# Performance work log

Hardware: AMD Instinct MI355X
Metric: run time of the kernel (lower is better)

Reference implementation:

```python
import jax, jax.numpy as jnp
import numpy as np

D = 256          # in_dim == out_dim for both layers
B, S = 8, 1024   # batch, seq_len
EPS = 1e-5       # LayerNorm eps (torch default)


def _layernorm(x, g, b):
    mu = jnp.mean(x, axis=-1, keepdims=True)
    var = jnp.var(x, axis=-1, keepdims=True)
    return (x - mu) * jax.lax.rsqrt(var + EPS) * g + b


def _periods(d):
    i = jnp.arange(d, dtype=jnp.float32)
    # periods[i, j] = i*d + j + 2
    return i[:, None] * d + i[None, :] + 2.0


def _layer(x, M, P, g, b, positions):
    # x: [B, S, in_dim] -> [B, S, out_dim]
    x_trans = jnp.einsum('bsj,ij->bsi', x, M)      # x @ M.T
    x_trans = _layernorm(x_trans, g, b)
    k = positions.astype(jnp.float32)[:, None, None]            # [S,1,1]
    phi = jnp.cos(2.0 * jnp.pi * k / _periods(D)[None])         # [S,D,D]
    Mk = P[None] * phi                                          # [S,D,D]
    Nk = jnp.einsum('bsj,sij->bsi', x_trans, Mk)
    # use_residual='separate' with in_dim==out_dim -> Identity residual
    return Nk + x


def setup_inputs() -> dict:
    key = jax.random.key(0)
    ks = jax.random.split(key, 5)
    seq = jax.random.normal(ks[0], (B, S, D), dtype=jnp.float32)
    M1 = jax.random.uniform(ks[1], (D, D), jnp.float32, -0.5, 0.5)
    P1 = jax.random.uniform(ks[2], (D, D), jnp.float32, -0.1, 0.1)
    M2 = jax.random.uniform(ks[3], (D, D), jnp.float32, -0.5, 0.5)
    P2 = jax.random.uniform(ks[4], (D, D), jnp.float32, -0.1, 0.1)
    g1 = jnp.ones((D,), jnp.float32); b1 = jnp.zeros((D,), jnp.float32)
    g2 = jnp.ones((D,), jnp.float32); b2 = jnp.zeros((D,), jnp.float32)
    return {"seq": seq, "M1": M1, "P1": P1, "g1": g1, "b1": b1,
            "M2": M2, "P2": P2, "g2": g2, "b2": b2}


def reference(seq, M1, P1, g1, b1, M2, P2, g2, b2):
    positions = jnp.arange(S)
    x = _layer(seq, M1, P1, g1, b1, positions)
    x = _layer(x, M2, P2, g2, b2, positions)
    return x
```

## Files before the change

kernel.cpp:

```cpp
#include <hip/hip_runtime.h>

#define DD 256
#define BB 8
#define SS 1024
#define XSTRIDE 264
#define RSTRIDE 260

#define LAYER_BYTES 262144
#define PTAB_OFF    131072
#define WS_NEEDED   (2 * LAYER_BYTES)

typedef _Float16 half8  __attribute__((ext_vector_type(8)));
typedef _Float16 half2t __attribute__((ext_vector_type(2)));
typedef __fp16   fp16x2 __attribute__((ext_vector_type(2)));
typedef __attribute__((ext_vector_type(4))) float float4v;

union h8u { half8 h; half2t h2[4]; };

__device__ __forceinline__ half2t pkrtz(float a, float b) {
    union { fp16x2 f; half2t h; } cv;
    cv.f = __builtin_amdgcn_cvt_pkrtz(a, b);
    return cv.h;
}

__device__ __forceinline__ float cosrev(float x) {
    return __builtin_amdgcn_cosf(__builtin_amdgcn_fractf(x));
}

__global__ void build_tabs(const float* __restrict__ M1, const float* __restrict__ P1,
                           const float* __restrict__ M2, const float* __restrict__ P2,
                           char* __restrict__ ws)
{
    int gid   = blockIdx.x * 256 + threadIdx.x;
    int layer = gid >> 13;
    int gi    = gid & 8191;
    int idx   = gi >> 6;
    int lane  = gi & 63;
    int wt    = idx & 15;
    int l15   = lane & 15, quad = lane >> 4;
    int kt    = idx >> 4;
    int n     = 16 * wt + l15;
    int j0    = kt * 32 + quad * 8;

    const float* Msrc = layer ? M2 : M1;
    const float* Psrc = layer ? P2 : P1;

    h8u mh, ph;
    #pragma unroll
    for (int e = 0; e < 4; ++e) {
        float ma = Msrc[(size_t)n * DD + j0 + 2 * e];
        float mb = Msrc[(size_t)n * DD + j0 + 2 * e + 1];
        float pa = Psrc[(size_t)n * DD + j0 + 2 * e];
        float pb = Psrc[(size_t)n * DD + j0 + 2 * e + 1];
        mh.h2[e] = pkrtz(ma, mb);
        ph.h2[e] = pkrtz(pa, pb);
    }
    char* base = ws + (size_t)layer * LAYER_BYTES;
    ((half8*)base)[gi]              = mh.h;
    ((half8*)(base + PTAB_OFF))[gi] = ph.h;
}

template<bool TABS>
__global__ __launch_bounds__(512, 4)
void fused_hierddpm(const float* __restrict__ seq,
                    const float* __restrict__ M1, const float* __restrict__ P1,
                    const float* __restrict__ g1, const float* __restrict__ be1,
                    const float* __restrict__ M2, const float* __restrict__ P2,
                    const float* __restrict__ g2, const float* __restrict__ be2,
                    const char* __restrict__ ws,
                    float* __restrict__ out)
{
    __shared__ __align__(16) _Float16 xsb[16][XSTRIDE];
    __shared__ __align__(16) _Float16 xtb[16][XSTRIDE];
    __shared__ __align__(16) float2 stats[16][8];
    __shared__ __align__(16) float res_lds[16][RSTRIDE];

    const int tid  = threadIdx.x;
    const int w    = tid >> 6;
    const int lane = tid & 63;
    const int l15  = lane & 15;
    const int quad = lane >> 4;
    const int s0   = blockIdx.x * 2;
    const float k0 = (float)s0;

    {
        const float4* seq4 = (const float4*)seq;
        #pragma unroll
        for (int u = 0; u < 2; ++u) {
            int v  = tid + 512 * u;
            int sl = v >> 9;
            int rm = v & 511;
            int b  = rm >> 6, j4 = rm & 63;
            float4 x = seq4[((size_t)b * SS + s0 + sl) * 64 + j4];
            int r = sl * 8 + b;
            half2t* dst = (half2t*)&xsb[r][4 * j4];
            dst[0] = pkrtz(x.x, x.y);
            dst[1] = pkrtz(x.z, x.w);
            *(float4*)&res_lds[r][4 * j4] = x;
        }
    }
    __syncthreads();

    #pragma unroll 1
    for (int layer = 0; layer < 2; ++layer) {
        const float* M  = layer ? M2  : M1;
        const float* P  = layer ? P2  : P1;
        const float* g  = layer ? g2  : g1;
        const float* be = layer ? be2 : be1;
        const char*  lbase = ws + (size_t)layer * LAYER_BYTES;
        const half8* Mtab = (const half8*)lbase;
        const half8* Ptab = (const half8*)(lbase + PTAB_OFF);

        float4v acc1[2];
        acc1[0] = (float4v){0.f, 0.f, 0.f, 0.f};
        acc1[1] = (float4v){0.f, 0.f, 0.f, 0.f};

        half8 aN = *(const half8*)&xsb[l15][quad * 8];
        half8 b0N, b1N;
        if (TABS) {
            b0N = Mtab[(2 * w) * 64 + lane];
            b1N = Mtab[(2 * w + 1) * 64 + lane];
        }
        #pragma unroll 1
        for (int kt = 0; kt < 8; ++kt) {
            half8 aC = aN;
            half8 b0C, b1C;
            if (TABS) {
                b0C = b0N; b1C = b1N;
            } else {
                #pragma unroll
                for (int t = 0; t < 2; ++t) {
                    int n = 16 * (2 * w + t) + l15;
                    const float4* Mr = (const float4*)M + ((size_t)n * 64 + kt * 8 + quad * 2);
                    float4 m0 = Mr[0], m1 = Mr[1];
                    h8u bb2;
                    bb2.h2[0] = pkrtz(m0.x, m0.y);
                    bb2.h2[1] = pkrtz(m0.z, m0.w);
                    bb2.h2[2] = pkrtz(m1.x, m1.y);
                    bb2.h2[3] = pkrtz(m1.z, m1.w);
                    if (t == 0) b0C = bb2.h; else b1C = bb2.h;
                }
            }
            if (kt < 7) {
                aN = *(const half8*)&xsb[l15][(kt + 1) * 32 + quad * 8];
                if (TABS) {
                    b0N = Mtab[((kt + 1) * 16 + 2 * w) * 64 + lane];
                    b1N = Mtab[((kt + 1) * 16 + 2 * w + 1) * 64 + lane];
                }
            }
            acc1[0] = __builtin_amdgcn_mfma_f32_16x16x32_f16(aC, b0C, acc1[0], 0, 0, 0);
            acc1[1] = __builtin_amdgcn_mfma_f32_16x16x32_f16(aC, b1C, acc1[1], 0, 0, 0);
        }

        half8 p0N, p1N;
        if (TABS) {
            p0N = Ptab[(2 * w) * 64 + lane];
            p1N = Ptab[(2 * w + 1) * 64 + lane];
        }

        #pragma unroll
        for (int reg = 0; reg < 4; ++reg) {
            float v0 = acc1[0][reg], v1 = acc1[1][reg];
            float sm = v0 + v1;
            float sq = fmaf(v0, v0, v1 * v1);
            #pragma unroll
            for (int off = 1; off < 16; off <<= 1) {
                sm += __shfl_xor(sm, off, 64);
                sq += __shfl_xor(sq, off, 64);
            }
            if (l15 == 0) stats[quad * 4 + reg][w] = make_float2(sm, sq);
        }
        __syncthreads();
        {
            int c0i = 16 * (2 * w) + l15, c1i = 16 * (2 * w + 1) + l15;
            float gv0 = g[c0i], bv0 = be[c0i];
            float gv1 = g[c1i], bv1 = be[c1i];
            #pragma unroll
            for (int reg = 0; reg < 4; ++reg) {
                int m = quad * 4 + reg;
                const float4* s4 = (const float4*)&stats[m][0];
                float4 q0 = s4[0], q1 = s4[1], q2 = s4[2], q3 = s4[3];
                float sm = (q0.x + q0.z) + (q1.x + q1.z) + (q2.x + q2.z) + (q3.x + q3.z);
                float sq = (q0.y + q0.w) + (q1.y + q1.w) + (q2.y + q2.w) + (q3.y + q3.w);
                float mm = sm * (1.f / DD);
                float rs = rsqrtf(sq * (1.f / DD) - mm * mm + 1e-5f);
                xtb[m][c0i] = (_Float16)fmaf((acc1[0][reg] - mm) * rs, gv0, bv0);
                xtb[m][c1i] = (_Float16)fmaf((acc1[1][reg] - mm) * rs, gv1, bv1);
            }
        }
        __syncthreads();

        float4v accS[2][2];
        #pragma unroll
        for (int k = 0; k < 2; ++k)
            #pragma unroll
            for (int t = 0; t < 2; ++t) accS[k][t] = (float4v){0.f, 0.f, 0.f, 0.f};

        float fb0 = (float)((16 * (2 * w) + l15) * DD + quad * 8 + 2);
        float fb1 = fb0 + 16.0f * DD;
        half8 aBN = *(const half8*)&xtb[l15][quad * 8];

        #pragma unroll 1
        for (int kt = 0; kt < 8; ++kt) {
            half8 aC = aBN;
            h8u p0C, p1C;
            if (TABS) {
                p0C.h = p0N; p1C.h = p1N;
            } else {
                #pragma unroll
                for (int t = 0; t < 2; ++t) {
                    int n = 16 * (2 * w + t) + l15;
                    const float4* Pr = (const float4*)P + ((size_t)n * 64 + kt * 8 + quad * 2);
                    float4 p0 = Pr[0], p1 = Pr[1];
                    h8u pv;
                    pv.h2[0] = pkrtz(p0.x, p0.y);
                    pv.h2[1] = pkrtz(p0.z, p0.w);
                    pv.h2[2] = pkrtz(p1.x, p1.y);
                    pv.h2[3] = pkrtz(p1.z, p1.w);
                    if (t == 0) p0C = pv; else p1C = pv;
                }
            }
            if (kt < 7) {
                aBN = *(const half8*)&xtb[l15][(kt + 1) * 32 + quad * 8];
                if (TABS) {
                    p0N = Ptab[((kt + 1) * 16 + 2 * w) * 64 + lane];
                    p1N = Ptab[((kt + 1) * 16 + 2 * w + 1) * 64 + lane];
                }
            }
            {
                h8u bA, bB;
                #pragma unroll
                for (int e = 0; e < 4; ++e) {
                    float ia = __builtin_amdgcn_rcpf(fb0 + (float)(2 * e));
                    float ib = __builtin_amdgcn_rcpf(fb0 + (float)(2 * e + 1));
                    float a0 = k0 * ia, b0f = k0 * ib;
                    float a1 = a0 + ia, b1f = b0f + ib;
                    half2t c0 = pkrtz(cosrev(a0), cosrev(b0f));
                    half2t c1 = pkrtz(cosrev(a1), cosrev(b1f));
                    bA.h2[e] = p0C.h2[e] * c0;
                    bB.h2[e] = p0C.h2[e] * c1;
                }
                accS[0][0] = __builtin_amdgcn_mfma_f32_16x16x32_f16(aC, bA.h, accS[0][0], 0, 0, 0);
                accS[1][0] = __builtin_amdgcn_mfma_f32_16x16x32_f16(aC, bB.h, accS[1][0], 0, 0, 0);
                fb0 += 32.0f;
            }
            {
                h8u bA, bB;
                #pragma unroll
                for (int e = 0; e < 4; ++e) {
                    float ia = __builtin_amdgcn_rcpf(fb1 + (float)(2 * e));
                    float ib = __builtin_amdgcn_rcpf(fb1 + (float)(2 * e + 1));
                    float a0 = k0 * ia, b0f = k0 * ib;
                    float a1 = a0 + ia, b1f = b0f + ib;
                    half2t c0 = pkrtz(cosrev(a0), cosrev(b0f));
                    half2t c1 = pkrtz(cosrev(a1), cosrev(b1f));
                    bA.h2[e] = p1C.h2[e] * c0;
                    bB.h2[e] = p1C.h2[e] * c1;
                }
                accS[0][1] = __builtin_amdgcn_mfma_f32_16x16x32_f16(aC, bA.h, accS[0][1], 0, 0, 0);
                accS[1][1] = __builtin_amdgcn_mfma_f32_16x16x32_f16(aC, bB.h, accS[1][1], 0, 0, 0);
                fb1 += 32.0f;
            }
        }

        #pragma unroll
        for (int t = 0; t < 2; ++t) {
            int col = 16 * (2 * w + t) + l15;
            float4v av = (quad < 2) ? accS[0][t] : accS[1][t];
            int sl = quad >> 1;
            #pragma unroll
            for (int reg = 0; reg < 4; ++reg) {
                int m = quad * 4 + reg;
                int b = m & 7;
                float val = av[reg] + res_lds[m][col];
                if (layer == 0) {
                    res_lds[m][col] = val;
                    xsb[m][col] = (_Float16)val;
                } else {
                    out[((size_t)b * SS + s0 + sl) * DD + col] = val;
                }
            }
        }
        if (layer == 0) __syncthreads();
    }
}

extern "C" void kernel_launch(void* const* d_in, const int* in_sizes, int n_in,
                              void* d_out, int out_size, void* d_ws, size_t ws_size,
                              hipStream_t stream)
{
    const float* seq = (const float*)d_in[0];
    const float* M1  = (const float*)d_in[1];
    const float* P1  = (const float*)d_in[2];
    const float* g1  = (const float*)d_in[3];
    const float* b1  = (const float*)d_in[4];
    const float* M2  = (const float*)d_in[5];
    const float* P2  = (const float*)d_in[6];
    const float* g2  = (const float*)d_in[7];
    const float* b2  = (const float*)d_in[8];
    float* out = (float*)d_out;

    if (ws_size >= WS_NEEDED) {
        build_tabs<<<64, 256, 0, stream>>>(M1, P1, M2, P2, (char*)d_ws);
        fused_hierddpm<true><<<SS / 2, 512, 0, stream>>>(
            seq, M1, P1, g1, b1, M2, P2, g2, b2, (const char*)d_ws, out);
    } else {
        fused_hierddpm<false><<<SS / 2, 512, 0, stream>>>(
            seq, M1, P1, g1, b1, M2, P2, g2, b2, nullptr, out);
    }
}
```

Measured before the change: 117.2 us.

## Split fused two-layer kernel into per-layer launches with output-column halves

Replaces the single fused two-layer kernel with one launch per layer. Each launch uses twice as many blocks, and each block computes only half of the output columns for the second matmul. The first matmul and the LayerNorm are computed redundantly in both column-half blocks, and the intermediate activation goes through global memory in the workspace. The aim is to double the number of blocks and raise occupancy, since launch bounds go from 4 to 8 and shared memory is smaller, so the cos-heavy second stage is spread across more CUs. The costs are an extra kernel launch, an extra global round-trip for the intermediate, and duplicated first-stage work.

Result: slower. 127.6 us (+8.9%).

```diff
diff --git a/kernel.cpp b/kernel.cpp
--- a/kernel.cpp
+++ b/kernel.cpp
@@ -4,11 +4,13 @@
 #define BB 8
 #define SS 1024
 #define XSTRIDE 264
-#define RSTRIDE 260
+#define RSTRIDE 132
 
 #define LAYER_BYTES 262144
 #define PTAB_OFF    131072
-#define WS_NEEDED   (2 * LAYER_BYTES)
+#define Y1_OFF      (2 * LAYER_BYTES)
+#define Y1_BYTES    (BB * SS * DD * 4)
+#define WS_NEEDED   (Y1_OFF + Y1_BYTES)
 
 typedef _Float16 half8  __attribute__((ext_vector_type(8)));
 typedef _Float16 half2t __attribute__((ext_vector_type(2)));
@@ -60,20 +62,162 @@
     ((half8*)(base + PTAB_OFF))[gi] = ph.h;
 }
 
-template<bool TABS>
+__global__ __launch_bounds__(512, 8)
+void split_layer(const float* __restrict__ src,
+                 const char*  __restrict__ lbase,
+                 const float* __restrict__ g,
+                 const float* __restrict__ be,
+                 float* __restrict__ dst)
+{
+    __shared__ __align__(16) _Float16 xsb[16][XSTRIDE];
+    __shared__ __align__(16) _Float16 xtb[16][XSTRIDE];
+    __shared__ __align__(16) float2 stats[16][8];
+    __shared__ __align__(16) float res_lds[16][RSTRIDE];
+
+    const half8* Mtab = (const half8*)lbase;
+    const half8* Ptab = (const half8*)(lbase + PTAB_OFF);
+
+    const int tid  = threadIdx.x;
+    const int w    = tid >> 6;
+    const int lane = tid & 63;
+    const int l15  = lane & 15;
+    const int quad = lane >> 4;
+    const int sp   = blockIdx.x >> 1;
+    const int ch   = blockIdx.x & 1;
+    const int s0   = sp * 2;
+    const float k0 = (float)s0;
+
+    {
+        const float4* src4 = (const float4*)src;
+        #pragma unroll
+        for (int u = 0; u < 2; ++u) {
+            int v  = tid + 512 * u;
+            int sl = v >> 9;
+            int rm = v & 511;
+            int b  = rm >> 6, j4 = rm & 63;
+            float4 x = src4[((size_t)b * SS + s0 + sl) * 64 + j4];
+            int r = sl * 8 + b;
+            half2t* d2 = (half2t*)&xsb[r][4 * j4];
+            d2[0] = pkrtz(x.x, x.y);
+            d2[1] = pkrtz(x.z, x.w);
+            if ((j4 >> 5) == ch)
+                *(float4*)&res_lds[r][4 * (j4 & 31)] = x;
+        }
+    }
+    __syncthreads();
+
+    float4v acc1[2];
+    acc1[0] = (float4v){0.f, 0.f, 0.f, 0.f};
+    acc1[1] = (float4v){0.f, 0.f, 0.f, 0.f};
+
+    half8 aN  = *(const half8*)&xsb[l15][quad * 8];
+    half8 b0N = Mtab[(2 * w) * 64 + lane];
+    half8 b1N = Mtab[(2 * w + 1) * 64 + lane];
+    #pragma unroll 1
+    for (int kt = 0; kt < 8; ++kt) {
+        half8 aC = aN, b0C = b0N, b1C = b1N;
+        if (kt < 7) {
+            aN  = *(const half8*)&xsb[l15][(kt + 1) * 32 + quad * 8];
+            b0N = Mtab[((kt + 1) * 16 + 2 * w) * 64 + lane];
+            b1N = Mtab[((kt + 1) * 16 + 2 * w + 1) * 64 + lane];
+        }
+        acc1[0] = __builtin_amdgcn_mfma_f32_16x16x32_f16(aC, b0C, acc1[0], 0, 0, 0);
+        acc1[1] = __builtin_amdgcn_mfma_f32_16x16x32_f16(aC, b1C, acc1[1], 0, 0, 0);
+    }
+
+    half8 pN = Ptab[(ch * 8 + w) * 64 + lane];
+
+    #pragma unroll
+    for (int reg = 0; reg < 4; ++reg) {
+        float v0 = acc1[0][reg], v1 = acc1[1][reg];
+        float sm = v0 + v1;
+        float sq = fmaf(v0, v0, v1 * v1);
+        #pragma unroll
+        for (int off = 1; off < 16; off <<= 1) {
+            sm += __shfl_xor(sm, off, 64);
+            sq += __shfl_xor(sq, off, 64);
+        }
+        if (l15 == 0) stats[quad * 4 + reg][w] = make_float2(sm, sq);
+    }
+    __syncthreads();
+    {
+        int c0i = 16 * (2 * w) + l15, c1i = 16 * (2 * w + 1) + l15;
+        float gv0 = g[c0i], bv0 = be[c0i];
+        float gv1 = g[c1i], bv1 = be[c1i];
+        #pragma unroll
+        for (int reg = 0; reg < 4; ++reg) {
+            int m = quad * 4 + reg;
+            const float4* s4 = (const float4*)&stats[m][0];
+            float4 q0 = s4[0], q1 = s4[1], q2 = s4[2], q3 = s4[3];
+            float sm = (q0.x + q0.z) + (q1.x + q1.z) + (q2.x + q2.z) + (q3.x + q3.z);
+            float sq = (q0.y + q0.w) + (q1.y + q1.w) + (q2.y + q2.w) + (q3.y + q3.w);
+            float mm = sm * (1.f / DD);
+            float rs = rsqrtf(sq * (1.f / DD) - mm * mm + 1e-5f);
+            xtb[m][c0i] = (_Float16)fmaf((acc1[0][reg] - mm) * rs, gv0, bv0);
+            xtb[m][c1i] = (_Float16)fmaf((acc1[1][reg] - mm) * rs, gv1, bv1);
+        }
+    }
+    __syncthreads();
+
+    float4v accS[2];
+    accS[0] = (float4v){0.f, 0.f, 0.f, 0.f};
+    accS[1] = (float4v){0.f, 0.f, 0.f, 0.f};
+
+    const int nB = 16 * (ch * 8 + w) + l15;
+    float fb = (float)(nB * DD + quad * 8 + 2);
+    half8 aBN = *(const half8*)&xtb[l15][quad * 8];
+
+    #pragma unroll 1
+    for (int kt = 0; kt < 8; ++kt) {
+        half8 aC = aBN;
+        h8u pC; pC.h = pN;
+        if (kt < 7) {
+            aBN = *(const half8*)&xtb[l15][(kt + 1) * 32 + quad * 8];
+            pN  = Ptab[((kt + 1) * 16 + ch * 8 + w) * 64 + lane];
+        }
+        h8u bA, bB;
+        #pragma unroll
+        for (int e = 0; e < 4; ++e) {
+            float ia = __builtin_amdgcn_rcpf(fb + (float)(2 * e));
+            float ib = __builtin_amdgcn_rcpf(fb + (float)(2 * e + 1));
+            float a0 = k0 * ia, b0f = k0 * ib;
+            float a1 = a0 + ia, b1f = b0f + ib;
+            half2t c0 = pkrtz(cosrev(a0), cosrev(b0f));
+            half2t c1 = pkrtz(cosrev(a1), cosrev(b1f));
+            bA.h2[e] = pC.h2[e] * c0;
+            bB.h2[e] = pC.h2[e] * c1;
+        }
+        accS[0] = __builtin_amdgcn_mfma_f32_16x16x32_f16(aC, bA.h, accS[0], 0, 0, 0);
+        accS[1] = __builtin_amdgcn_mfma_f32_16x16x32_f16(aC, bB.h, accS[1], 0, 0, 0);
+        fb += 32.0f;
+    }
+
+    {
+        int col = nB;
+        int cl  = 16 * w + l15;
+        float4v av = (quad < 2) ? accS[0] : accS[1];
+        int sl = quad >> 1;
+        #pragma unroll
+        for (int reg = 0; reg < 4; ++reg) {
+            int m = quad * 4 + reg;
+            int b = m & 7;
+            dst[((size_t)b * SS + s0 + sl) * DD + col] = av[reg] + res_lds[m][cl];
+        }
+    }
+}
+
 __global__ __launch_bounds__(512, 4)
-void fused_hierddpm(const float* __restrict__ seq,
+void fused_fallback(const float* __restrict__ seq,
                     const float* __restrict__ M1, const float* __restrict__ P1,
                     const float* __restrict__ g1, const float* __restrict__ be1,
                     const float* __restrict__ M2, const float* __restrict__ P2,
                     const float* __restrict__ g2, const float* __restrict__ be2,
-                    const char* __restrict__ ws,
                     float* __restrict__ out)
 {
     __shared__ __align__(16) _Float16 xsb[16][XSTRIDE];
     __shared__ __align__(16) _Float16 xtb[16][XSTRIDE];
     __shared__ __align__(16) float2 stats[16][8];
-    __shared__ __align__(16) float res_lds[16][RSTRIDE];
+    __shared__ __align__(16) float res_lds[16][2 * RSTRIDE];
 
     const int tid  = threadIdx.x;
     const int w    = tid >> 6;
@@ -93,9 +237,9 @@
             int b  = rm >> 6, j4 = rm & 63;
             float4 x = seq4[((size_t)b * SS + s0 + sl) * 64 + j4];
             int r = sl * 8 + b;
-            half2t* dst = (half2t*)&xsb[r][4 * j4];
-            dst[0] = pkrtz(x.x, x.y);
-            dst[1] = pkrtz(x.z, x.w);
+            half2t* d2 = (half2t*)&xsb[r][4 * j4];
+            d2[0] = pkrtz(x.x, x.y);
+            d2[1] = pkrtz(x.z, x.w);
             *(float4*)&res_lds[r][4 * j4] = x;
         }
     }
@@ -107,55 +251,26 @@
         const float* P  = layer ? P2  : P1;
         const float* g  = layer ? g2  : g1;
         const float* be = layer ? be2 : be1;
-        const char*  lbase = ws + (size_t)layer * LAYER_BYTES;
-        const half8* Mtab = (const half8*)lbase;
-        const half8* Ptab = (const half8*)(lbase + PTAB_OFF);
 
         float4v acc1[2];
         acc1[0] = (float4v){0.f, 0.f, 0.f, 0.f};
         acc1[1] = (float4v){0.f, 0.f, 0.f, 0.f};
 
-        half8 aN = *(const half8*)&xsb[l15][quad * 8];
-        half8 b0N, b1N;
-        if (TABS) {
-            b0N = Mtab[(2 * w) * 64 + lane];
-            b1N = Mtab[(2 * w + 1) * 64 + lane];
-        }
         #pragma unroll 1
         for (int kt = 0; kt < 8; ++kt) {
-            half8 aC = aN;
-            half8 b0C, b1C;
-            if (TABS) {
-                b0C = b0N; b1C = b1N;
-            } else {
-                #pragma unroll
-                for (int t = 0; t < 2; ++t) {
-                    int n = 16 * (2 * w + t) + l15;
-                    const float4* Mr = (const float4*)M + ((size_t)n * 64 + kt * 8 + quad * 2);
-                    float4 m0 = Mr[0], m1 = Mr[1];
-                    h8u bb2;
-                    bb2.h2[0] = pkrtz(m0.x, m0.y);
-                    bb2.h2[1] = pkrtz(m0.z, m0.w);
-                    bb2.h2[2] = pkrtz(m1.x, m1.y);
-                    bb2.h2[3] = pkrtz(m1.z, m1.w);
-                    if (t == 0) b0C = bb2.h; else b1C = bb2.h;
-                }
-            }
-            if (kt < 7) {
-                aN = *(const half8*)&xsb[l15][(kt + 1) * 32 + quad * 8];
-                if (TABS) {
-                    b0N = Mtab[((kt + 1) * 16 + 2 * w) * 64 + lane];
-                    b1N = Mtab[((kt + 1) * 16 + 2 * w + 1) * 64 + lane];
-                }
-            }
-            acc1[0] = __builtin_amdgcn_mfma_f32_16x16x32_f16(aC, b0C, acc1[0], 0, 0, 0);
-            acc1[1] = __builtin_amdgcn_mfma_f32_16x16x32_f16(aC, b1C, acc1[1], 0, 0, 0);
-        }
-
-        half8 p0N, p1N;
-        if (TABS) {
-            p0N = Ptab[(2 * w) * 64 + lane];
-            p1N = Ptab[(2 * w + 1) * 64 + lane];
+            half8 a = *(const half8*)&xsb[l15][kt * 32 + quad * 8];
+            #pragma unroll
+            for (int t = 0; t < 2; ++t) {
+                int n = 16 * (2 * w + t) + l15;
+                const float4* Mr = (const float4*)M + ((size_t)n * 64 + kt * 8 + quad * 2);
+                float4 m0 = Mr[0], m1 = Mr[1];
+                h8u bb2;
+                bb2.h2[0] = pkrtz(m0.x, m0.y);
+                bb2.h2[1] = pkrtz(m0.z, m0.w);
+                bb2.h2[2] = pkrtz(m1.x, m1.y);
+                bb2.h2[3] = pkrtz(m1.z, m1.w);
+                acc1[t] = __builtin_amdgcn_mfma_f32_16x16x32_f16(a, bb2.h, acc1[t], 0, 0, 0);
+            }
         }
 
         #pragma unroll
@@ -198,69 +313,37 @@
 
         float fb0 = (float)((16 * (2 * w) + l15) * DD + quad * 8 + 2);
         float fb1 = fb0 + 16.0f * DD;
-        half8 aBN = *(const half8*)&xtb[l15][quad * 8];
 
         #pragma unroll 1
         for (int kt = 0; kt < 8; ++kt) {
-            half8 aC = aBN;
-            h8u p0C, p1C;
-            if (TABS) {
-                p0C.h = p0N; p1C.h = p1N;
-            } else {
-                #pragma unroll
-                for (int t = 0; t < 2; ++t) {
-                    int n = 16 * (2 * w + t) + l15;
-                    const float4* Pr = (const float4*)P + ((size_t)n * 64 + kt * 8 + quad * 2);
-                    float4 p0 = Pr[0], p1 = Pr[1];
-                    h8u pv;
-                    pv.h2[0] = pkrtz(p0.x, p0.y);
-                    pv.h2[1] = pkrtz(p0.z, p0.w);
-                    pv.h2[2] = pkrtz(p1.x, p1.y);
-                    pv.h2[3] = pkrtz(p1.z, p1.w);
-                    if (t == 0) p0C = pv; else p1C = pv;
-                }
-            }
-            if (kt < 7) {
-                aBN = *(const half8*)&xtb[l15][(kt + 1) * 32 + quad * 8];
-                if (TABS) {
-                    p0N = Ptab[((kt + 1) * 16 + 2 * w) * 64 + lane];
-                    p1N = Ptab[((kt + 1) * 16 + 2 * w + 1) * 64 + lane];
-                }
-            }
-            {
+            half8 a = *(const half8*)&xtb[l15][kt * 32 + quad * 8];
+            #pragma unroll
+            for (int t = 0; t < 2; ++t) {
+                int n = 16 * (2 * w + t) + l15;
+                const float4* Pr = (const float4*)P + ((size_t)n * 64 + kt * 8 + quad * 2);
+                float4 p0 = Pr[0], p1 = Pr[1];
+                h8u pv;
+                pv.h2[0] = pkrtz(p0.x, p0.y);
+                pv.h2[1] = pkrtz(p0.z, p0.w);
+                pv.h2[2] = pkrtz(p1.x, p1.y);
+                pv.h2[3] = pkrtz(p1.z, p1.w);
+                float fb = (t == 0) ? fb0 : fb1;
                 h8u bA, bB;
                 #pragma unroll
                 for (int e = 0; e < 4; ++e) {
-                    float ia = __builtin_amdgcn_rcpf(fb0 + (float)(2 * e));
-                    float ib = __builtin_amdgcn_rcpf(fb0 + (float)(2 * e + 1));
+                    float ia = __builtin_amdgcn_rcpf(fb + (float)(2 * e));
+                    float ib = __builtin_amdgcn_rcpf(fb + (float)(2 * e + 1));
                     float a0 = k0 * ia, b0f = k0 * ib;
                     float a1 = a0 + ia, b1f = b0f + ib;
                     half2t c0 = pkrtz(cosrev(a0), cosrev(b0f));
                     half2t c1 = pkrtz(cosrev(a1), cosrev(b1f));
-                    bA.h2[e] = p0C.h2[e] * c0;
-                    bB.h2[e] = p0C.h2[e] * c1;
+                    bA.h2[e] = pv.h2[e] * c0;
+                    bB.h2[e] = pv.h2[e] * c1;
                 }
-                accS[0][0] = __builtin_amdgcn_mfma_f32_16x16x32_f16(aC, bA.h, accS[0][0], 0, 0, 0);
-                accS[1][0] = __builtin_amdgcn_mfma_f32_16x16x32_f16(aC, bB.h, accS[1][0], 0, 0, 0);
-                fb0 += 32.0f;
-            }
-            {
-                h8u bA, bB;
-                #pragma unroll
-                for (int e = 0; e < 4; ++e) {
-                    float ia = __builtin_amdgcn_rcpf(fb1 + (float)(2 * e));
-                    float ib = __builtin_amdgcn_rcpf(fb1 + (float)(2 * e + 1));
-                    float a0 = k0 * ia, b0f = k0 * ib;
-                    float a1 = a0 + ia, b1f = b0f + ib;
-                    half2t c0 = pkrtz(cosrev(a0), cosrev(b0f));
-                    half2t c1 = pkrtz(cosrev(a1), cosrev(b1f));
-                    bA.h2[e] = p1C.h2[e] * c0;
-                    bB.h2[e] = p1C.h2[e] * c1;
-                }
-                accS[0][1] = __builtin_amdgcn_mfma_f32_16x16x32_f16(aC, bA.h, accS[0][1], 0, 0, 0);
-                accS[1][1] = __builtin_amdgcn_mfma_f32_16x16x32_f16(aC, bB.h, accS[1][1], 0, 0, 0);
-                fb1 += 32.0f;
-            }
+                accS[0][t] = __builtin_amdgcn_mfma_f32_16x16x32_f16(a, bA.h, accS[0][t], 0, 0, 0);
+                accS[1][t] = __builtin_amdgcn_mfma_f32_16x16x32_f16(a, bB.h, accS[1][t], 0, 0, 0);
+            }
+            fb0 += 32.0f; fb1 += 32.0f;
         }
 
         #pragma unroll
@@ -301,11 +384,13 @@
     float* out = (float*)d_out;
 
     if (ws_size >= WS_NEEDED) {
-        build_tabs<<<64, 256, 0, stream>>>(M1, P1, M2, P2, (char*)d_ws);
-        fused_hierddpm<true><<<SS / 2, 512, 0, stream>>>(
-            seq, M1, P1, g1, b1, M2, P2, g2, b2, (const char*)d_ws, out);
+        char* ws = (char*)d_ws;
+        float* y1 = (float*)(ws + Y1_OFF);
+        build_tabs<<<64, 256, 0, stream>>>(M1, P1, M2, P2, ws);
+        split_layer<<<SS, 512, 0, stream>>>(seq, ws, g1, b1, y1);
+        split_layer<<<SS, 512, 0, stream>>>(y1, ws + LAYER_BYTES, g2, b2, out);
     } else {
-        fused_hierddpm<false><<<SS / 2, 512, 0, stream>>>(
-            seq, M1, P1, g1, b1, M2, P2, g2, b2, nullptr, out);
-    }
-}
+        fused_fallback<<<SS / 2, 512, 0, stream>>>(
+            seq, M1, P1, g1, b1, M2, P2, g2, b2, out);
+    }
+}
```

## Process one sequence position per block and drop fract for small cosine arguments

Applied to the files above, without the earlier changes.

Each block now handles one sequence position instead of two, so the grid doubles to 1024 blocks and the launch bound rises to 8 blocks per SM. MFMA tiles are padded by repeating the 8 batch rows into the 16-row A operand, and results are written only for the valid half. The cosine factors are now computed once per position, so reciprocals are no longer shared across two positions. Register prefetching of the A and B fragments is removed. For waves whose period guarantees an argument below one revolution, the fract step before the hardware cosine is skipped. In exchange, half of the MFMA work is wasted on padded rows, reciprocal work doubles in total, and the loops lose their explicit load/compute overlap.

After: 116.5 us. About the same (-0.6%).

```diff
diff --git a/kernel.cpp b/kernel.cpp
--- a/kernel.cpp
+++ b/kernel.cpp
@@ -25,6 +25,9 @@
 
 __device__ __forceinline__ float cosrev(float x) {
     return __builtin_amdgcn_cosf(__builtin_amdgcn_fractf(x));
+}
+__device__ __forceinline__ float cosq(float x) {
+    return __builtin_amdgcn_cosf(x);
 }
 
 __global__ void build_tabs(const float* __restrict__ M1, const float* __restrict__ P1,
@@ -61,7 +64,7 @@
 }
 
 template<bool TABS>
-__global__ __launch_bounds__(512, 4)
+__global__ __launch_bounds__(512, 8)
 void fused_hierddpm(const float* __restrict__ seq,
                     const float* __restrict__ M1, const float* __restrict__ P1,
                     const float* __restrict__ g1, const float* __restrict__ be1,
@@ -70,34 +73,28 @@
                     const char* __restrict__ ws,
                     float* __restrict__ out)
 {
-    __shared__ __align__(16) _Float16 xsb[16][XSTRIDE];
-    __shared__ __align__(16) _Float16 xtb[16][XSTRIDE];
-    __shared__ __align__(16) float2 stats[16][8];
-    __shared__ __align__(16) float res_lds[16][RSTRIDE];
+    __shared__ __align__(16) _Float16 xsb[8][XSTRIDE];
+    __shared__ __align__(16) _Float16 xtb[8][XSTRIDE];
+    __shared__ __align__(16) float2 stats[8][8];
+    __shared__ __align__(16) float res_lds[8][RSTRIDE];
 
     const int tid  = threadIdx.x;
     const int w    = tid >> 6;
     const int lane = tid & 63;
     const int l15  = lane & 15;
+    const int l7   = l15 & 7;
     const int quad = lane >> 4;
-    const int s0   = blockIdx.x * 2;
-    const float k0 = (float)s0;
+    const int s    = blockIdx.x;
+    const float k0 = (float)s;
 
     {
         const float4* seq4 = (const float4*)seq;
-        #pragma unroll
-        for (int u = 0; u < 2; ++u) {
-            int v  = tid + 512 * u;
-            int sl = v >> 9;
-            int rm = v & 511;
-            int b  = rm >> 6, j4 = rm & 63;
-            float4 x = seq4[((size_t)b * SS + s0 + sl) * 64 + j4];
-            int r = sl * 8 + b;
-            half2t* dst = (half2t*)&xsb[r][4 * j4];
-            dst[0] = pkrtz(x.x, x.y);
-            dst[1] = pkrtz(x.z, x.w);
-            *(float4*)&res_lds[r][4 * j4] = x;
-        }
+        int row = tid >> 6, j4 = tid & 63;
+        float4 x = seq4[((size_t)row * SS + s) * 64 + j4];
+        half2t* dst = (half2t*)&xsb[row][4 * j4];
+        dst[0] = pkrtz(x.x, x.y);
+        dst[1] = pkrtz(x.z, x.w);
+        *(float4*)&res_lds[row][4 * j4] = x;
     }
     __syncthreads();
 
@@ -115,21 +112,15 @@
         acc1[0] = (float4v){0.f, 0.f, 0.f, 0.f};
         acc1[1] = (float4v){0.f, 0.f, 0.f, 0.f};
 
-        half8 aN = *(const half8*)&xsb[l15][quad * 8];
-        half8 b0N, b1N;
-        if (TABS) {
-            b0N = Mtab[(2 * w) * 64 + lane];
-            b1N = Mtab[(2 * w + 1) * 64 + lane];
-        }
         #pragma unroll 1
         for (int kt = 0; kt < 8; ++kt) {
-            half8 aC = aN;
-            half8 b0C, b1C;
-            if (TABS) {
-                b0C = b0N; b1C = b1N;
-            } else {
-                #pragma unroll
-                for (int t = 0; t < 2; ++t) {
+            half8 a = *(const half8*)&xsb[l7][kt * 32 + quad * 8];
+            #pragma unroll
+            for (int t = 0; t < 2; ++t) {
+                half8 bf;
+                if (TABS) {
+                    bf = Mtab[(kt * 16 + 2 * w + t) * 64 + lane];
+                } else {
                     int n = 16 * (2 * w + t) + l15;
                     const float4* Mr = (const float4*)M + ((size_t)n * 64 + kt * 8 + quad * 2);
                     float4 m0 = Mr[0], m1 = Mr[1];
@@ -138,24 +129,10 @@
                     bb2.h2[1] = pkrtz(m0.z, m0.w);
                     bb2.h2[2] = pkrtz(m1.x, m1.y);
                     bb2.h2[3] = pkrtz(m1.z, m1.w);
-                    if (t == 0) b0C = bb2.h; else b1C = bb2.h;
-                }
-            }
-            if (kt < 7) {
-                aN = *(const half8*)&xsb[l15][(kt + 1) * 32 + quad * 8];
-                if (TABS) {
-                    b0N = Mtab[((kt + 1) * 16 + 2 * w) * 64 + lane];
-                    b1N = Mtab[((kt + 1) * 16 + 2 * w + 1) * 64 + lane];
-                }
-            }
-            acc1[0] = __builtin_amdgcn_mfma_f32_16x16x32_f16(aC, b0C, acc1[0], 0, 0, 0);
-            acc1[1] = __builtin_amdgcn_mfma_f32_16x16x32_f16(aC, b1C, acc1[1], 0, 0, 0);
-        }
-
-        half8 p0N, p1N;
-        if (TABS) {
-            p0N = Ptab[(2 * w) * 64 + lane];
-            p1N = Ptab[(2 * w + 1) * 64 + lane];
+                    bf = bb2.h;
+                }
+                acc1[t] = __builtin_amdgcn_mfma_f32_16x16x32_f16(a, bf, acc1[t], 0, 0, 0);
+            }
         }
 
         #pragma unroll
@@ -168,11 +145,11 @@
                 sm += __shfl_xor(sm, off, 64);
                 sq += __shfl_xor(sq, off, 64);
             }
-            if (l15 == 0) stats[quad * 4 + reg][w] = make_float2(sm, sq);
+            if (l15 == 0 && quad < 2) stats[quad * 4 + reg][w] = make_float2(sm, sq);
         }
         __syncthreads();
-        {
-            int c0i = 16 * (2 * w) + l15, c1i = 16 * (2 * w + 1) + l15;
+        if (quad < 2) {
+            int c0i = 16 * (2 * w) + l15, c1i = c0i + 16;
             float gv0 = g[c0i], bv0 = be[c0i];
             float gv1 = g[c1i], bv1 = be[c1i];
             #pragma unroll
@@ -190,94 +167,87 @@
         }
         __syncthreads();
 
-        float4v accS[2][2];
-        #pragma unroll
-        for (int k = 0; k < 2; ++k)
-            #pragma unroll
-            for (int t = 0; t < 2; ++t) accS[k][t] = (float4v){0.f, 0.f, 0.f, 0.f};
+        float4v accS[2];
+        accS[0] = (float4v){0.f, 0.f, 0.f, 0.f};
+        accS[1] = (float4v){0.f, 0.f, 0.f, 0.f};
 
         float fb0 = (float)((16 * (2 * w) + l15) * DD + quad * 8 + 2);
         float fb1 = fb0 + 16.0f * DD;
-        half8 aBN = *(const half8*)&xtb[l15][quad * 8];
 
         #pragma unroll 1
         for (int kt = 0; kt < 8; ++kt) {
-            half8 aC = aBN;
-            h8u p0C, p1C;
-            if (TABS) {
-                p0C.h = p0N; p1C.h = p1N;
-            } else {
-                #pragma unroll
-                for (int t = 0; t < 2; ++t) {
-                    int n = 16 * (2 * w + t) + l15;
+            half8 a = *(const half8*)&xtb[l7][kt * 32 + quad * 8];
+            {
+                h8u pC;
+                if (TABS) {
+                    pC.h = Ptab[(kt * 16 + 2 * w) * 64 + lane];
+                } else {
+                    int n = 16 * (2 * w) + l15;
                     const float4* Pr = (const float4*)P + ((size_t)n * 64 + kt * 8 + quad * 2);
                     float4 p0 = Pr[0], p1 = Pr[1];
-                    h8u pv;
-                    pv.h2[0] = pkrtz(p0.x, p0.y);
-                    pv.h2[1] = pkrtz(p0.z, p0.w);
-                    pv.h2[2] = pkrtz(p1.x, p1.y);
-                    pv.h2[3] = pkrtz(p1.z, p1.w);
-                    if (t == 0) p0C = pv; else p1C = pv;
-                }
-            }
-            if (kt < 7) {
-                aBN = *(const half8*)&xtb[l15][(kt + 1) * 32 + quad * 8];
+                    pC.h2[0] = pkrtz(p0.x, p0.y);
+                    pC.h2[1] = pkrtz(p0.z, p0.w);
+                    pC.h2[2] = pkrtz(p1.x, p1.y);
+                    pC.h2[3] = pkrtz(p1.z, p1.w);
+                }
+                h8u bA;
+                if (w == 0) {
+                    #pragma unroll
+                    for (int e = 0; e < 4; ++e) {
+                        float ia = __builtin_amdgcn_rcpf(fb0 + (float)(2 * e));
+                        float ib = __builtin_amdgcn_rcpf(fb0 + (float)(2 * e + 1));
+                        bA.h2[e] = pC.h2[e] * pkrtz(cosrev(k0 * ia), cosrev(k0 * ib));
+                    }
+                } else {
+                    #pragma unroll
+                    for (int e = 0; e < 4; ++e) {
+                        float ia = __builtin_amdgcn_rcpf(fb0 + (float)(2 * e));
+                        float ib = __builtin_amdgcn_rcpf(fb0 + (float)(2 * e + 1));
+                        bA.h2[e] = pC.h2[e] * pkrtz(cosq(k0 * ia), cosq(k0 * ib));
+                    }
+                }
+                accS[0] = __builtin_amdgcn_mfma_f32_16x16x32_f16(a, bA.h, accS[0], 0, 0, 0);
+                fb0 += 32.0f;
+            }
+            {
+                h8u pC;
                 if (TABS) {
-                    p0N = Ptab[((kt + 1) * 16 + 2 * w) * 64 + lane];
-                    p1N = Ptab[((kt + 1) * 16 + 2 * w + 1) * 64 + lane];
-                }
-            }
-            {
-                h8u bA, bB;
-                #pragma unroll
-                for (int e = 0; e < 4; ++e) {
-                    float ia = __builtin_amdgcn_rcpf(fb0 + (float)(2 * e));
-                    float ib = __builtin_amdgcn_rcpf(fb0 + (float)(2 * e + 1));
-                    float a0 = k0 * ia, b0f = k0 * ib;
-                    float a1 = a0 + ia, b1f = b0f + ib;
-                    half2t c0 = pkrtz(cosrev(a0), cosrev(b0f));
-                    half2t c1 = pkrtz(cosrev(a1), cosrev(b1f));
-                    bA.h2[e] = p0C.h2[e] * c0;
-                    bB.h2[e] = p0C.h2[e] * c1;
-                }
-                accS[0][0] = __builtin_amdgcn_mfma_f32_16x16x32_f16(aC, bA.h, accS[0][0], 0, 0, 0);
-                accS[1][0] = __builtin_amdgcn_mfma_f32_16x16x32_f16(aC, bB.h, accS[1][0], 0, 0, 0);
-                fb0 += 32.0f;
-            }
-            {
-                h8u bA, bB;
+                    pC.h = Ptab[(kt * 16 + 2 * w + 1) * 64 + lane];
+                } else {
+                    int n = 16 * (2 * w + 1) + l15;
+                    const float4* Pr = (const float4*)P + ((size_t)n * 64 + kt * 8 + quad * 2);
+                    float4 p0 = Pr[0], p1 = Pr[1];
+                    pC.h2[0] = pkrtz(p0.x, p0.y);
+                    pC.h2[1] = pkrtz(p0.z, p0.w);
+                    pC.h2[2] = pkrtz(p1.x, p1.y);
+                    pC.h2[3] = pkrtz(p1.z, p1.w);
+                }
+                h8u bB;
                 #pragma unroll
                 for (int e = 0; e < 4; ++e) {
                     float ia = __builtin_amdgcn_rcpf(fb1 + (float)(2 * e));
                     float ib = __builtin_amdgcn_rcpf(fb1 + (float)(2 * e + 1));
-                    float a0 = k0 * ia, b0f = k0 * ib;
-                    float a1 = a0 + ia, b1f = b0f + ib;
-                    half2t c0 = pkrtz(cosrev(a0), cosrev(b0f));
-                    half2t c1 = pkrtz(cosrev(a1), cosrev(b1f));
-                    bA.h2[e] = p1C.h2[e] * c0;
-                    bB.h2[e] = p1C.h2[e] * c1;
-                }
-                accS[0][1] = __builtin_amdgcn_mfma_f32_16x16x32_f16(aC, bA.h, accS[0][1], 0, 0, 0);
-                accS[1][1] = __builtin_amdgcn_mfma_f32_16x16x32_f16(aC, bB.h, accS[1][1], 0, 0, 0);
+                    bB.h2[e] = pC.h2[e] * pkrtz(cosq(k0 * ia), cosq(k0 * ib));
+                }
+                accS[1] = __builtin_amdgcn_mfma_f32_16x16x32_f16(a, bB.h, accS[1], 0, 0, 0);
                 fb1 += 32.0f;
             }
         }
 
-        #pragma unroll
-        for (int t = 0; t < 2; ++t) {
-            int col = 16 * (2 * w + t) + l15;
-            float4v av = (quad < 2) ? accS[0][t] : accS[1][t];
-            int sl = quad >> 1;
-            #pragma unroll
-            for (int reg = 0; reg < 4; ++reg) {
-                int m = quad * 4 + reg;
-                int b = m & 7;
-                float val = av[reg] + res_lds[m][col];
-                if (layer == 0) {
-                    res_lds[m][col] = val;
-                    xsb[m][col] = (_Float16)val;
-                } else {
-                    out[((size_t)b * SS + s0 + sl) * DD + col] = val;
+        if (quad < 2) {
+            #pragma unroll
+            for (int t = 0; t < 2; ++t) {
+                int col = 16 * (2 * w + t) + l15;
+                #pragma unroll
+                for (int reg = 0; reg < 4; ++reg) {
+                    int m = quad * 4 + reg;
+                    float val = accS[t][reg] + res_lds[m][col];
+                    if (layer == 0) {
+                        res_lds[m][col] = val;
+                        xsb[m][col] = (_Float16)val;
+                    } else {
+                        out[((size_t)m * SS + s) * DD + col] = val;
+                    }
                 }
             }
         }
@@ -302,10 +272,10 @@
 
     if (ws_size >= WS_NEEDED) {
         build_tabs<<<64, 256, 0, stream>>>(M1, P1, M2, P2, (char*)d_ws);
-        fused_hierddpm<true><<<SS / 2, 512, 0, stream>>>(
+        fused_hierddpm<true><<<SS, 512, 0, stream>>>(
             seq, M1, P1, g1, b1, M2, P2, g2, b2, (const char*)d_ws, out);
     } else {
-        fused_hierddpm<false><<<SS / 2, 512, 0, stream>>>(
+        fused_hierddpm<false><<<SS, 512, 0, stream>>>(
             seq, M1, P1, g1, b1, M2, P2, g2, b2, nullptr, out);
     }
 }
```
